# Kernel tuning notes

Measured on AMD Instinct MI355X. Metric: run time of the kernel, lower is better.

## Reference

```python
import jax, jax.numpy as jnp
import numpy as np

B, T, N, F = 4, 12, 4096, 32
NG = 14  # 14 gate GNNs: fx,fh,ix,ih,cx,ch,ox,oh,i,im,g,gm,o,om


def setup_inputs() -> dict:
    key = jax.random.key(0)
    k1, k2, k3 = jax.random.split(key, 3)
    x = jax.random.normal(k1, (B, T, N, F), dtype=jnp.float32)
    # weighted adjacency, scaled like row-normalized so adj@x stays O(1)
    adj = jax.random.uniform(k2, (B, N, N), dtype=jnp.float32) / N
    W = jax.random.normal(k3, (NG, F, 2 * F), dtype=jnp.float32) * (1.0 / np.sqrt(F))
    b = jnp.zeros((NG, 2 * F), dtype=jnp.float32)
    return {"x": x, "adj": adj, "W": W, "b": b}


def _wgc(v, adj, Wi, bi):
    # WeightedGraphConv: adj-matmul -> Dense(2F) -> GLU
    y = jnp.matmul(adj, v)                 # [B,N,F]
    z = jnp.matmul(y, Wi) + bi             # [B,N,2F]
    ls, rs = jnp.split(z, 2, axis=-1)
    return ls * jax.nn.sigmoid(rs)         # [B,N,F]


def reference(x, adj, W, b):
    Bb, Tt, Nn, Ff = x.shape
    ones = jnp.ones((Bb, Nn, Ff), dtype=x.dtype)
    h0, c0, m0 = ones, ones, ones

    def step(carry, xt):
        h, c, m = carry
        g = lambda i, v: _wgc(v, adj, W[i], b[i])
        f = jax.nn.sigmoid(g(0, xt) + g(1, h))     # forget
        i = jax.nn.sigmoid(g(2, xt) + g(3, h))     # input
        o = jax.nn.sigmoid(g(6, xt) + g(7, h))     # output
        c_new = f * c + i * jnp.tanh(g(4, xt) + g(5, h))
        h_mid = o * jnp.tanh(c_new)
        # memory-state gates (has_memory_state=True)
        i2 = jax.nn.sigmoid(g(8, h_mid) + g(9, m))
        gg = jax.nn.sigmoid(g(10, h_mid) + g(11, m))
        o2 = jax.nn.sigmoid(g(12, h_mid) + g(13, m))
        m_new = i2 * m + (1.0 - i2) * gg
        h_new = m_new * o2
        return (h_new, c_new, m_new), h_new

    (last_h, last_c, last_m), hs = jax.lax.scan(step, (h0, c0, m0), jnp.swapaxes(x, 0, 1))
    hidden_states = jnp.swapaxes(hs, 0, 1)  # [B,T,N,F]
    return hidden_states, last_h, last_c, last_m
```

## Files before the change

kernel.cpp:

```cpp
#include <hip/hip_runtime.h>


typedef __bf16 bf16_t;
typedef __bf16 bf16x8 __attribute__((ext_vector_type(8)));
typedef float  f32x4  __attribute__((ext_vector_type(4)));

#define DI __device__ __forceinline__

#define BB 4
#define TT 12
#define NN 4096
#define FF 32

DI float sigm(float x)  { return __builtin_amdgcn_rcpf(1.f + __expf(-x)); }
DI float tanh_f(float x){ float e = __expf(2.f * x); return 1.f - 2.f * __builtin_amdgcn_rcpf(e + 1.f); }

__global__ __launch_bounds__(256) void conv_adj_k(const float* __restrict__ a,
                                                  bf16_t* __restrict__ o) {
    size_t i = ((size_t)blockIdx.x * 256 + threadIdx.x) * 8;
    float4 v0 = *(const float4*)(a + i);
    float4 v1 = *(const float4*)(a + i + 4);
    union { uint4 u; bf16_t h[8]; } t;
    t.h[0] = (bf16_t)v0.x; t.h[1] = (bf16_t)v0.y; t.h[2] = (bf16_t)v0.z; t.h[3] = (bf16_t)v0.w;
    t.h[4] = (bf16_t)v1.x; t.h[5] = (bf16_t)v1.y; t.h[6] = (bf16_t)v1.z; t.h[7] = (bf16_t)v1.w;
    *(uint4*)(o + i) = t.u;
}

__global__ __launch_bounds__(256) void xpose_k(const float* __restrict__ x,
                                               bf16_t* __restrict__ xT) {
    const int b = blockIdx.z, t = blockIdx.y, n0 = blockIdx.x * 64;
    const int tid = threadIdx.x;
    __shared__ float tile[64][33];
    const float* src = x + (((size_t)(b * TT + t)) * NN + n0) * FF;
#pragma unroll
    for (int rr = 0; rr < 2; ++rr) {
        int idx = rr * 256 + tid;
        int row = idx >> 3, seg = idx & 7;
        float4 v = *(const float4*)(src + row * FF + seg * 4);
        tile[row][seg * 4 + 0] = v.x; tile[row][seg * 4 + 1] = v.y;
        tile[row][seg * 4 + 2] = v.z; tile[row][seg * 4 + 3] = v.w;
    }
    __syncthreads();
    const int f = tid >> 3, seg = tid & 7;
    union { uint4 u; bf16_t h[8]; } o;
#pragma unroll
    for (int j = 0; j < 8; ++j) o.h[j] = (bf16_t)tile[seg * 8 + j][f];
    *(uint4*)&xT[((size_t)(b * 384 + t * FF + f)) * NN + n0 + seg * 8] = o.u;
}

__global__ __launch_bounds__(256) void make_wfrag_k(const float* __restrict__ W,
                                                    bf16_t* __restrict__ Wf) {
    const int g = blockIdx.x, tid = threadIdx.x;
    const int ct = tid >> 6, lane = tid & 63;
    const int k0 = (lane >> 4) * 8, col = ct * 16 + (lane & 15);
    union { uint4 u; bf16_t h[8]; } t;
#pragma unroll
    for (int j = 0; j < 8; ++j) t.h[j] = (bf16_t)W[(g * 32 + k0 + j) * 64 + col];
    *(uint4*)&Wf[((g * 4 + ct) * 64 + lane) * 8] = t.u;
}

__global__ __launch_bounds__(256) void init_k(bf16_t* h_bf, bf16_t* hm_bf,
                                              float* c, float* m) {
    const int idx = blockIdx.x * 256 + threadIdx.x;
    const int b = idx >> 17, r = idx & 131071;
    h_bf[idx] = (bf16_t)1.f;
    hm_bf[(size_t)b * 262144 + 131072 + r] = (bf16_t)1.f;
    c[idx] = 1.f;
    m[idx] = 1.f;
}

template <bool ABF, int S, int BS0, int BS1>
__global__ __launch_bounds__(256, 4) void gemm_splitk(const void* __restrict__ Ap,
                                                      const bf16_t* __restrict__ p0,
                                                      const bf16_t* __restrict__ p1,
                                                      float* __restrict__ Yp) {
    const int b = blockIdx.z;
    const int row0 = blockIdx.x * 64;
    const int slice = blockIdx.y;
    const int tid = threadIdx.x, wave = tid >> 6, lane = tid & 63;
    const int mrow = lane & 15, quad = lane >> 4;
    __shared__ __align__(16) bf16_t Vs[64 * 256];
    const f32x4 zero = {0.f, 0.f, 0.f, 0.f};
    f32x4 acc[4];
#pragma unroll
    for (int i = 0; i < 4; ++i) acc[i] = zero;
    const int row = row0 + wave * 16 + mrow;
    const size_t arow = ((size_t)b << 24) + (size_t)row * NN;

    for (int stg = 0; stg < 4; ++stg) {
        const int k0 = slice * 1024 + stg * 256;
        bf16x8 af[8];
        if constexpr (ABF) {
            const bf16_t* ab = (const bf16_t*)Ap + arow + k0 + quad * 8;
#pragma unroll
            for (int s = 0; s < 8; ++s) af[s] = *(const bf16x8*)(ab + s * 32);
        } else {
            const float* ab = (const float*)Ap + arow + k0 + quad * 8;
#pragma unroll
            for (int s = 0; s < 8; ++s) {
                float4 v0 = *(const float4*)(ab + s * 32);
                float4 v1 = *(const float4*)(ab + s * 32 + 4);
                af[s][0] = (bf16_t)v0.x; af[s][1] = (bf16_t)v0.y;
                af[s][2] = (bf16_t)v0.z; af[s][3] = (bf16_t)v0.w;
                af[s][4] = (bf16_t)v1.x; af[s][5] = (bf16_t)v1.y;
                af[s][6] = (bf16_t)v1.z; af[s][7] = (bf16_t)v1.w;
            }
        }
#pragma unroll
        for (int rr = 0; rr < 8; ++rr) {
            const int idx = rr * 256 + tid;
            const int c = idx >> 5, ch = idx & 31;
            const bf16_t* src = (S < 64 && c >= S)
                ? p1 + ((size_t)b * BS1 + (c - S)) * NN
                : p0 + ((size_t)b * BS0 + c) * NN;
            *(uint4*)&Vs[c * 256 + (ch ^ (c & 7)) * 8] =
                *(const uint4*)(src + k0 + ch * 8);
        }
        __syncthreads();
#pragma unroll
        for (int s = 0; s < 8; ++s) {
#pragma unroll
            for (int ct = 0; ct < 4; ++ct) {
                const int c = ct * 16 + mrow;
                bf16x8 bfr = *(const bf16x8*)&Vs[c * 256 + (((s * 4 + quad) ^ (c & 7)) * 8)];
                acc[ct] = __builtin_amdgcn_mfma_f32_16x16x32_bf16(af[s], bfr, acc[ct], 0, 0, 0);
            }
        }
        __syncthreads();
    }
    float* dst = Yp + ((size_t)(b * 4 + slice) * NN) * 64;
#pragma unroll
    for (int ct = 0; ct < 4; ++ct) {
        const int col = ct * 16 + mrow;
#pragma unroll
        for (int r = 0; r < 4; ++r) {
            const int orow = row0 + wave * 16 + quad * 4 + r;
            dst[(size_t)orow * 64 + col] = acc[ct][r];
        }
    }
}

__global__ __launch_bounds__(256) void gates1_k(const float* __restrict__ Yp,
                                                const bf16_t* __restrict__ Wf,
                                                const float* __restrict__ bias,
                                                float* __restrict__ c,
                                                bf16_t* __restrict__ hm_bf) {
    const int b = blockIdx.y, n0 = blockIdx.x * 64;
    const int tid = threadIdx.x, wave = tid >> 6, lane = tid & 63;
    const int mrow = lane & 15, quad = lane >> 4;
    const int nw = n0 + wave * 16;
    const f32x4 zero = {0.f, 0.f, 0.f, 0.f};
    const float* ybase = Yp + ((size_t)b * 4 * NN + nw + mrow) * 64;
    f32x4 h0 = zero, h1 = zero, x0 = zero, x1 = zero;
#pragma unroll
    for (int sl = 0; sl < 4; ++sl) {
        const float* yr = ybase + (size_t)sl * NN * 64;
        h0 += *(const f32x4*)(yr + quad * 8);
        h1 += *(const f32x4*)(yr + quad * 8 + 4);
        x0 += *(const f32x4*)(yr + 32 + quad * 8);
        x1 += *(const f32x4*)(yr + 32 + quad * 8 + 4);
    }
    bf16x8 ah, ax;
#pragma unroll
    for (int j = 0; j < 4; ++j) {
        ah[j] = (bf16_t)h0[j]; ah[j + 4] = (bf16_t)h1[j];
        ax[j] = (bf16_t)x0[j]; ax[j + 4] = (bf16_t)x1[j];
    }
    float gate[4][2][4];
#pragma unroll
    for (int gi = 0; gi < 4; ++gi) {
        const int ge = 2 * gi, go = ge + 1;
        f32x4 ze[4], zo[4];
#pragma unroll
        for (int ct = 0; ct < 4; ++ct) {
            bf16x8 we = *(const bf16x8*)&Wf[((ge * 4 + ct) * 64 + lane) * 8];
            bf16x8 wo = *(const bf16x8*)&Wf[((go * 4 + ct) * 64 + lane) * 8];
            ze[ct] = __builtin_amdgcn_mfma_f32_16x16x32_bf16(ax, we, zero, 0, 0, 0);
            zo[ct] = __builtin_amdgcn_mfma_f32_16x16x32_bf16(ah, wo, zero, 0, 0, 0);
            const float be = bias[ge * 64 + ct * 16 + mrow];
            const float bo = bias[go * 64 + ct * 16 + mrow];
#pragma unroll
            for (int r = 0; r < 4; ++r) { ze[ct][r] += be; zo[ct][r] += bo; }
        }
#pragma unroll
        for (int p = 0; p < 2; ++p)
#pragma unroll
            for (int r = 0; r < 4; ++r) {
                float s = ze[p][r] * sigm(ze[p + 2][r]) + zo[p][r] * sigm(zo[p + 2][r]);
                gate[gi][p][r] = (gi == 2) ? tanh_f(s) : sigm(s);
            }
    }
    __shared__ bf16_t hmT[32][64];
#pragma unroll
    for (int p = 0; p < 2; ++p)
#pragma unroll
        for (int r = 0; r < 4; ++r) {
            const int row = nw + quad * 4 + r, col = p * 16 + mrow;
            const size_t ci = ((size_t)b * NN + row) * FF + col;
            float cn = gate[0][p][r] * c[ci] + gate[1][p][r] * gate[2][p][r];
            c[ci] = cn;
            hmT[col][wave * 16 + quad * 4 + r] = (bf16_t)(gate[3][p][r] * tanh_f(cn));
        }
    __syncthreads();
    {
        const int col = tid >> 3, seg = tid & 7;
        union { uint4 u; bf16_t h[8]; } o;
#pragma unroll
        for (int j = 0; j < 8; ++j) o.h[j] = hmT[col][seg * 8 + j];
        *(uint4*)&hm_bf[((size_t)b * 64 + col) * NN + n0 + seg * 8] = o.u;
    }
}

__global__ __launch_bounds__(256) void gates2_k(const float* __restrict__ Yp,
                                                const bf16_t* __restrict__ Wf,
                                                const float* __restrict__ bias,
                                                float* __restrict__ m,
                                                bf16_t* __restrict__ hm_bf,
                                                bf16_t* __restrict__ h_bf,
                                                float* __restrict__ hs, int t) {
    const int b = blockIdx.y, n0 = blockIdx.x * 64;
    const int tid = threadIdx.x, wave = tid >> 6, lane = tid & 63;
    const int mrow = lane & 15, quad = lane >> 4;
    const int nw = n0 + wave * 16;
    const f32x4 zero = {0.f, 0.f, 0.f, 0.f};
    const float* ybase = Yp + ((size_t)b * 4 * NN + nw + mrow) * 64;
    f32x4 h0 = zero, h1 = zero, m0 = zero, m1 = zero;
#pragma unroll
    for (int sl = 0; sl < 4; ++sl) {
        const float* yr = ybase + (size_t)sl * NN * 64;
        h0 += *(const f32x4*)(yr + quad * 8);
        h1 += *(const f32x4*)(yr + quad * 8 + 4);
        m0 += *(const f32x4*)(yr + 32 + quad * 8);
        m1 += *(const f32x4*)(yr + 32 + quad * 8 + 4);
    }
    bf16x8 axh, axm;
#pragma unroll
    for (int j = 0; j < 4; ++j) {
        axh[j] = (bf16_t)h0[j]; axh[j + 4] = (bf16_t)h1[j];
        axm[j] = (bf16_t)m0[j]; axm[j + 4] = (bf16_t)m1[j];
    }
    float gate[3][2][4];
#pragma unroll
    for (int gi = 0; gi < 3; ++gi) {
        const int ge = 8 + 2 * gi, go = ge + 1;
        f32x4 ze[4], zo[4];
#pragma unroll
        for (int ct = 0; ct < 4; ++ct) {
            bf16x8 we = *(const bf16x8*)&Wf[((ge * 4 + ct) * 64 + lane) * 8];
            bf16x8 wo = *(const bf16x8*)&Wf[((go * 4 + ct) * 64 + lane) * 8];
            ze[ct] = __builtin_amdgcn_mfma_f32_16x16x32_bf16(axh, we, zero, 0, 0, 0);
            zo[ct] = __builtin_amdgcn_mfma_f32_16x16x32_bf16(axm, wo, zero, 0, 0, 0);
            const float be = bias[ge * 64 + ct * 16 + mrow];
            const float bo = bias[go * 64 + ct * 16 + mrow];
#pragma unroll
            for (int r = 0; r < 4; ++r) { ze[ct][r] += be; zo[ct][r] += bo; }
        }
#pragma unroll
        for (int p = 0; p < 2; ++p)
#pragma unroll
            for (int r = 0; r < 4; ++r) {
                float s = ze[p][r] * sigm(ze[p + 2][r]) + zo[p][r] * sigm(zo[p + 2][r]);
                gate[gi][p][r] = sigm(s);
            }
    }
    __shared__ bf16_t mT[32][64];
    __shared__ bf16_t hT[32][64];
#pragma unroll
    for (int p = 0; p < 2; ++p)
#pragma unroll
        for (int r = 0; r < 4; ++r) {
            const int row = nw + quad * 4 + r, col = p * 16 + mrow;
            const size_t ci = ((size_t)b * NN + row) * FF + col;
            const float i2 = gate[0][p][r], gg = gate[1][p][r], o2 = gate[2][p][r];
            float mn = i2 * m[ci] + (1.f - i2) * gg;
            m[ci] = mn;
            float hn = mn * o2;
            hs[(((size_t)b * TT + t) * NN + row) * FF + col] = hn;
            mT[col][wave * 16 + quad * 4 + r] = (bf16_t)mn;
            hT[col][wave * 16 + quad * 4 + r] = (bf16_t)hn;
        }
    __syncthreads();
    {
        const int col = tid >> 3, seg = tid & 7;
        union { uint4 u; bf16_t h[8]; } om, oh;
#pragma unroll
        for (int j = 0; j < 8; ++j) { om.h[j] = mT[col][seg * 8 + j]; oh.h[j] = hT[col][seg * 8 + j]; }
        *(uint4*)&hm_bf[((size_t)b * 64 + 32 + col) * NN + n0 + seg * 8] = om.u;
        *(uint4*)&h_bf[((size_t)b * FF + col) * NN + n0 + seg * 8] = oh.u;
    }
}

__global__ __launch_bounds__(256) void finalize_k(const float* __restrict__ hs,
                                                  const float* __restrict__ c,
                                                  const float* __restrict__ m,
                                                  float* __restrict__ tail) {
    const int idx = blockIdx.x * 256 + threadIdx.x;
    const int b = idx >> 17, r = idx & 131071;
    tail[idx] = hs[((size_t)b * TT + (TT - 1)) * 131072 + r];
    tail[524288 + idx] = c[idx];
    tail[1048576 + idx] = m[idx];
}

extern "C" void kernel_launch(void* const* d_in, const int* in_sizes, int n_in,
                              void* d_out, int out_size, void* d_ws, size_t ws_size,
                              hipStream_t stream) {
    const float* x    = (const float*)d_in[0];
    const float* adj  = (const float*)d_in[1];
    const float* W    = (const float*)d_in[2];
    const float* bias = (const float*)d_in[3];
    float* out = (float*)d_out;

    char* ws = (char*)d_ws;
    size_t off = 0;
    auto carve = [&](size_t bytes) -> void* {
        void* p = ws + off;
        off += (bytes + 255) & ~(size_t)255;
        return p;
    };
    bf16_t* xT    = (bf16_t*)carve((size_t)BB * 384 * NN * 2);
    float*  Yp    = (float*)carve((size_t)BB * 4 * NN * 64 * 4);
    bf16_t* h_bf  = (bf16_t*)carve((size_t)BB * FF * NN * 2);
    bf16_t* hm_bf = (bf16_t*)carve((size_t)BB * 64 * NN * 2);
    bf16_t* Wf    = (bf16_t*)carve((size_t)14 * 4 * 64 * 8 * 2);
    float*  cbuf  = (float*)carve((size_t)BB * NN * FF * 4);
    float*  mbuf  = (float*)carve((size_t)BB * NN * FF * 4);
    const size_t adj_bytes = (size_t)BB * NN * NN * 2;
    const bool abf = (ws_size >= off + adj_bytes);
    bf16_t* adj_bf = abf ? (bf16_t*)carve(adj_bytes) : nullptr;

    if (abf) conv_adj_k<<<32768, 256, 0, stream>>>(adj, adj_bf);
    make_wfrag_k<<<14, 256, 0, stream>>>(W, Wf);
    xpose_k<<<dim3(64, TT, BB), 256, 0, stream>>>(x, xT);
    init_k<<<2048, 256, 0, stream>>>(h_bf, hm_bf, cbuf, mbuf);

    const dim3 ggrid(64, 4, BB);
    for (int t = 0; t < TT; ++t) {
        const bf16_t* xts = xT + (size_t)t * 32 * NN;
        if (abf) gemm_splitk<true, 32, 32, 384><<<ggrid, 256, 0, stream>>>(adj_bf, h_bf, xts, Yp);
        else     gemm_splitk<false, 32, 32, 384><<<ggrid, 256, 0, stream>>>(adj, h_bf, xts, Yp);
        gates1_k<<<dim3(64, BB), 256, 0, stream>>>(Yp, Wf, bias, cbuf, hm_bf);
        if (abf) gemm_splitk<true, 64, 64, 64><<<ggrid, 256, 0, stream>>>(adj_bf, hm_bf, hm_bf, Yp);
        else     gemm_splitk<false, 64, 64, 64><<<ggrid, 256, 0, stream>>>(adj, hm_bf, hm_bf, Yp);
        gates2_k<<<dim3(64, BB), 256, 0, stream>>>(Yp, Wf, bias, mbuf, hm_bf, h_bf, out, t);
    }
    finalize_k<<<2048, 256, 0, stream>>>(out, cbuf, mbuf, out + (size_t)BB * TT * NN * FF);
}
```

Before: 1.309 ms.

## Software-pipeline split-K GEMM with register prefetch and smaller K stages

```diff
diff --git a/kernel.cpp b/kernel.cpp
--- a/kernel.cpp
+++ b/kernel.cpp
@@ -79,7 +79,7 @@
     const int slice = blockIdx.y;
     const int tid = threadIdx.x, wave = tid >> 6, lane = tid & 63;
     const int mrow = lane & 15, quad = lane >> 4;
-    __shared__ __align__(16) bf16_t Vs[64 * 256];
+    __shared__ __align__(16) bf16_t Vs[64 * 128];
     const f32x4 zero = {0.f, 0.f, 0.f, 0.f};
     f32x4 acc[4];
 #pragma unroll
@@ -87,47 +87,77 @@
     const int row = row0 + wave * 16 + mrow;
     const size_t arow = ((size_t)b << 24) + (size_t)row * NN;
 
-    for (int stg = 0; stg < 4; ++stg) {
-        const int k0 = slice * 1024 + stg * 256;
-        bf16x8 af[8];
+    const bf16_t* bsrc[4];
+    int ldst[4];
+#pragma unroll
+    for (int rr = 0; rr < 4; ++rr) {
+        const int idx = rr * 256 + tid;
+        const int c = idx >> 4, ch = idx & 15;
+        const bf16_t* srcrow = (S < 64 && c >= S)
+            ? p1 + ((size_t)b * BS1 + (c - S)) * NN
+            : p0 + ((size_t)b * BS0 + c) * NN;
+        bsrc[rr] = srcrow + slice * 1024 + ch * 8;
+        ldst[rr] = c * 128 + ((ch ^ (c & 7)) * 8);
+    }
+
+    const bf16_t* Abase  = (const bf16_t*)Ap + arow + slice * 1024 + quad * 8;
+    const float*  AbaseF = (const float*)Ap  + arow + slice * 1024 + quad * 8;
+
+    uint4  brg[4];
+    bf16x8 af[2][4];
+
+    auto loadB = [&](int stg) {
+#pragma unroll
+        for (int rr = 0; rr < 4; ++rr)
+            brg[rr] = *(const uint4*)(bsrc[rr] + stg * 128);
+    };
+    auto writeB = [&]() {
+#pragma unroll
+        for (int rr = 0; rr < 4; ++rr) *(uint4*)&Vs[ldst[rr]] = brg[rr];
+    };
+    auto loadA = [&](int buf, int stg) {
         if constexpr (ABF) {
-            const bf16_t* ab = (const bf16_t*)Ap + arow + k0 + quad * 8;
-#pragma unroll
-            for (int s = 0; s < 8; ++s) af[s] = *(const bf16x8*)(ab + s * 32);
+#pragma unroll
+            for (int s = 0; s < 4; ++s)
+                af[buf][s] = *(const bf16x8*)(Abase + stg * 128 + s * 32);
         } else {
-            const float* ab = (const float*)Ap + arow + k0 + quad * 8;
-#pragma unroll
-            for (int s = 0; s < 8; ++s) {
-                float4 v0 = *(const float4*)(ab + s * 32);
-                float4 v1 = *(const float4*)(ab + s * 32 + 4);
-                af[s][0] = (bf16_t)v0.x; af[s][1] = (bf16_t)v0.y;
-                af[s][2] = (bf16_t)v0.z; af[s][3] = (bf16_t)v0.w;
-                af[s][4] = (bf16_t)v1.x; af[s][5] = (bf16_t)v1.y;
-                af[s][6] = (bf16_t)v1.z; af[s][7] = (bf16_t)v1.w;
+#pragma unroll
+            for (int s = 0; s < 4; ++s) {
+                float4 v0 = *(const float4*)(AbaseF + stg * 128 + s * 32);
+                float4 v1 = *(const float4*)(AbaseF + stg * 128 + s * 32 + 4);
+                af[buf][s][0] = (bf16_t)v0.x; af[buf][s][1] = (bf16_t)v0.y;
+                af[buf][s][2] = (bf16_t)v0.z; af[buf][s][3] = (bf16_t)v0.w;
+                af[buf][s][4] = (bf16_t)v1.x; af[buf][s][5] = (bf16_t)v1.y;
+                af[buf][s][6] = (bf16_t)v1.z; af[buf][s][7] = (bf16_t)v1.w;
             }
         }
-#pragma unroll
-        for (int rr = 0; rr < 8; ++rr) {
-            const int idx = rr * 256 + tid;
-            const int c = idx >> 5, ch = idx & 31;
-            const bf16_t* src = (S < 64 && c >= S)
-                ? p1 + ((size_t)b * BS1 + (c - S)) * NN
-                : p0 + ((size_t)b * BS0 + c) * NN;
-            *(uint4*)&Vs[c * 256 + (ch ^ (c & 7)) * 8] =
-                *(const uint4*)(src + k0 + ch * 8);
-        }
-        __syncthreads();
-#pragma unroll
-        for (int s = 0; s < 8; ++s) {
+    };
+
+    loadB(0);
+    loadA(0, 0);
+    writeB();
+    __syncthreads();
+
+#pragma unroll
+    for (int stg = 0; stg < 8; ++stg) {
+        const int cur = stg & 1;
+        if (stg < 7) { loadB(stg + 1); loadA(cur ^ 1, stg + 1); }
+#pragma unroll
+        for (int s = 0; s < 4; ++s) {
 #pragma unroll
             for (int ct = 0; ct < 4; ++ct) {
                 const int c = ct * 16 + mrow;
-                bf16x8 bfr = *(const bf16x8*)&Vs[c * 256 + (((s * 4 + quad) ^ (c & 7)) * 8)];
-                acc[ct] = __builtin_amdgcn_mfma_f32_16x16x32_bf16(af[s], bfr, acc[ct], 0, 0, 0);
+                bf16x8 bfr = *(const bf16x8*)&Vs[c * 128 + (((s * 4 + quad) ^ (c & 7)) * 8)];
+                acc[ct] = __builtin_amdgcn_mfma_f32_16x16x32_bf16(af[cur][s], bfr, acc[ct], 0, 0, 0);
             }
         }
-        __syncthreads();
-    }
+        if (stg < 7) {
+            __syncthreads();
+            writeB();
+            __syncthreads();
+        }
+    }
+
     float* dst = Yp + ((size_t)(b * 4 + slice) * NN) * 64;
 #pragma unroll
     for (int ct = 0; ct < 4; ++ct) {
```

New measurement: 1.885 ms. +44.0%, slower.
